# Kernel optimization log

Measured on AMD Instinct MI355X. Metric: run time of the kernel, lower is better.

Reference implementation:

```python
import jax, jax.numpy as jnp
import numpy as np

B, H, W, DIM, NH = 4, 32, 32, 768, 12
HD = DIM // NH  # head_dim = 64


def setup_inputs() -> dict:
    key = jax.random.key(0)
    ks = jax.random.split(key, 12)
    n = lambda i, shape, s=1.0: jax.random.normal(ks[i], shape, jnp.float32) * s
    return {
        "q": n(0, (B, H, W, DIM)),
        "k": n(1, (B, H, W, DIM)),
        "v": n(2, (B, H, W, DIM)),
        # Linear weights stored as (in, out) so y = x @ W + b (equivalent to torch x @ W.T)
        "Wq": n(3, (DIM, DIM), 0.02), "bq": jnp.zeros((DIM,), jnp.float32),
        "Wk": n(4, (DIM, DIM), 0.02), "bk": jnp.zeros((DIM,), jnp.float32),
        "Wv": n(5, (DIM, DIM), 0.02), "bv": jnp.zeros((DIM,), jnp.float32),
        "Wp": n(6, (DIM, DIM), 0.02), "bp": jnp.zeros((DIM,), jnp.float32),
        # decomposed relative position tables: (2*size - 1, head_dim)
        "rel_pos_h": n(7, (2 * H - 1, HD), 0.02),
        "rel_pos_w": n(8, (2 * W - 1, HD), 0.02),
    }


def reference(q, k, v, Wq, bq, Wk, bk, Wv, bv, Wp, bp, rel_pos_h, rel_pos_w):
    scale = HD ** -0.5

    def to_heads(x, Wt, b):
        y = x.reshape(B, H * W, DIM) @ Wt + b          # (B, HW, DIM)
        return y.reshape(B, H * W, NH, HD).transpose(0, 2, 1, 3).reshape(B * NH, H * W, HD)

    qh = to_heads(q, Wq, bq)   # (B*NH, HW, HD)
    kh = to_heads(k, Wk, bk)
    vh = to_heads(v, Wv, bv)

    # scaled dot-product scores
    attn = jnp.einsum('bqd,bkd->bqk', qh * scale, kh)  # (B*NH, HW, HW)

    # decomposed relative position bias (q_size == k_size == input_size, no interpolation)
    idx_h = jnp.arange(H)[:, None] - jnp.arange(H)[None, :] + (H - 1)
    idx_w = jnp.arange(W)[:, None] - jnp.arange(W)[None, :] + (W - 1)
    Rh = rel_pos_h[idx_h]  # (H, H, HD)
    Rw = rel_pos_w[idx_w]  # (W, W, HD)
    rq = qh.reshape(B * NH, H, W, HD)  # unscaled q, as in torch add_decomposed_rel_pos
    rel_h = jnp.einsum('bhwc,hkc->bhwk', rq, Rh)  # (B*NH, H, W, H)
    rel_w = jnp.einsum('bhwc,wkc->bhwk', rq, Rw)  # (B*NH, H, W, W)

    attn = (attn.reshape(B * NH, H, W, H, W)
            + rel_h[:, :, :, :, None]
            + rel_w[:, :, :, None, :]).reshape(B * NH, H * W, H * W)

    attn = jax.nn.softmax(attn, axis=-1)
    x = (attn @ vh).reshape(B, NH, H, W, HD).transpose(0, 2, 3, 1, 4).reshape(B, H, W, DIM)
    return x @ Wp + bp
```

## Files before the change

kernel.cpp:

```cpp
#include <hip/hip_runtime.h>
#include <math.h>

#define DIM  768
#define NH   12
#define HD   64
#define HWN  1024
#define MROWS 4096

typedef __attribute__((ext_vector_type(8))) short short8;
typedef __attribute__((ext_vector_type(4))) float f32x4;
typedef _Float16 h8 __attribute__((ext_vector_type(8)));
typedef _Float16 h2 __attribute__((ext_vector_type(2)));

__device__ __forceinline__ void gl_lds16(const void* g, void* l) {
    __builtin_amdgcn_global_load_lds(
        (const __attribute__((address_space(1))) void*)g,
        (__attribute__((address_space(3))) void*)l, 16, 0, 0);
}

__global__ __launch_bounds__(256) void xconv_kernel(
    const float* __restrict__ q, const float* __restrict__ k,
    const float* __restrict__ v, _Float16* __restrict__ xf16)
{
    const int N8 = MROWS * DIM / 8;
    int i = blockIdx.x * 256 + threadIdx.x;
    const int stride = gridDim.x * 256;
    for (; i < 3 * N8; i += stride) {
        const int sel = i / N8, j = i - sel * N8;
        const float* src = (sel == 0) ? q : (sel == 1) ? k : v;
        float4 a0 = ((const float4*)src)[j * 2];
        float4 a1 = ((const float4*)src)[j * 2 + 1];
        h8 o = {(_Float16)a0.x, (_Float16)a0.y, (_Float16)a0.z, (_Float16)a0.w,
                (_Float16)a1.x, (_Float16)a1.y, (_Float16)a1.z, (_Float16)a1.w};
        *(h8*)(xf16 + (size_t)sel * (MROWS * DIM) + (size_t)j * 8) = o;
    }
}

__global__ __launch_bounds__(256) void wconv_kernel(
    const float* __restrict__ Wq, const float* __restrict__ Wk,
    const float* __restrict__ Wv, const float* __restrict__ Wp,
    _Float16* __restrict__ WtAll)
{
    __shared__ float Ws[64][65];
    const int z = blockIdx.z;
    const float* W = (z == 0) ? Wq : (z == 1) ? Wk : (z == 2) ? Wv : Wp;
    _Float16* Wt = WtAll + (size_t)z * 589824;

    const int k0 = blockIdx.y * 64, n0 = blockIdx.x * 64;
    const int t = threadIdx.x;
    {
        int r = t >> 2, c4 = (t & 3) * 16;
        #pragma unroll
        for (int u = 0; u < 16; u += 4)
            *(float4*)&Ws[r][c4 + u] = *(const float4*)(W + (size_t)(k0 + r) * DIM + n0 + c4 + u);
    }
    __syncthreads();
    const int n = t >> 2, kseg = (t & 3) * 16;
    h8 h0, h1;
    #pragma unroll
    for (int j = 0; j < 8; ++j) {
        h0[j] = (_Float16)Ws[kseg + j][n];
        h1[j] = (_Float16)Ws[kseg + 8 + j][n];
    }
    size_t base = (size_t)(n0 + n) * DIM + k0 + kseg;
    *(h8*)(Wt + base) = h0;
    *(h8*)(Wt + base + 8) = h1;
}

__global__ __launch_bounds__(256) void rel2frag_kernel(
    const float* __restrict__ rph, const float* __restrict__ rpw,
    _Float16* __restrict__ relTg)
{
    const int t = threadIdx.x;
    const int row = t >> 1, c0 = (t & 1) * 32;
    const float* src = (row < 63) ? rph + (size_t)row * HD
                     : (row >= 64 && row < 127) ? rpw + (size_t)(row - 64) * HD
                     : nullptr;
    #pragma unroll
    for (int g = 0; g < 4; ++g) {
        h8 o;
        #pragma unroll
        for (int j = 0; j < 8; ++j)
            o[j] = src ? (_Float16)src[c0 + g * 8 + j] : (_Float16)0.0f;
        *(h8*)(relTg + (size_t)row * HD + c0 + g * 8) = o;
    }
}

template<int AMODE>
__global__ __launch_bounds__(256, 3) void gemm_mfma_kernel(
    const _Float16* __restrict__ X0, const _Float16* __restrict__ WtAll,
    const float* __restrict__ bias0, const float* __restrict__ bias1,
    const float* __restrict__ bias2,
    void* __restrict__ Y0, void* __restrict__ Y1, void* __restrict__ Y2)
{
    constexpr int MT = (AMODE == 0) ? 128 : 64;
    constexpr int RF = MT / 32;
    __shared__ __align__(16) char smem[MT * 128 + 12 * 1024];
    constexpr int BOFF = MT * 128;

    const int t = threadIdx.x;
    const int w = t >> 6, lane = t & 63;
    const int l15 = lane & 15, l4 = lane >> 4;

    int sel, rb, cb;
    if (AMODE == 0) {
        const int sw = (blockIdx.x & 7) * 96 + (blockIdx.x >> 3);
        sel = sw >> 8;
        const int rem = sw & 255;
        rb = rem >> 3; cb = rem & 7;
    } else {
        const int sw = (blockIdx.x & 7) * 64 + (blockIdx.x >> 3);
        sel = 3;
        rb = sw >> 3; cb = sw & 7;
    }
    const int row0 = rb * MT, col0 = cb * 96;

    const char* Ab = (const char*)(X0 + (AMODE == 0 ? (size_t)sel * (MROWS * DIM) : 0));
    const _Float16* Bt = WtAll + (size_t)sel * 589824;
    const float* bias = (AMODE == 1) ? bias0 : (sel == 0) ? bias0 : (sel == 1) ? bias1 : bias2;

    f32x4 acc[RF][3];
    #pragma unroll
    for (int i = 0; i < RF; ++i)
        #pragma unroll
        for (int j = 0; j < 3; ++j) acc[i][j] = (f32x4){0, 0, 0, 0};

    for (int kt = 0; kt < 12; ++kt) {
        #pragma unroll
        for (int i = 0; i < MT / 32; ++i) {
            const int fi = w * (MT / 32) + i;
            const int row = fi * 8 + (lane >> 3);
            const int srcb = ((lane & 7) * 16) ^ ((row & 7) << 4);
            gl_lds16(Ab + (size_t)(row0 + row) * 1536 + kt * 128 + srcb, smem + fi * 1024);
        }
        #pragma unroll
        for (int it = 0; it < 3; ++it) {
            const int f = it * 4 + w;
            const int ks = f / 6, cf = f % 6;
            const size_t off = (size_t)(col0 + cf * 16 + l15) * 1536 + kt * 128 + ks * 64 + l4 * 16;
            gl_lds16((const char*)Bt + off, smem + BOFF + f * 1024);
        }
        __syncthreads();

        __builtin_amdgcn_s_setprio(1);
        #pragma unroll
        for (int ks = 0; ks < 2; ++ks) {
            h8 b[3];
            #pragma unroll
            for (int cf4 = 0; cf4 < 3; ++cf4) {
                const int fb = ks * 6 + (w & 1) * 3 + cf4;
                b[cf4] = *(const h8*)(smem + BOFF + fb * 1024 + lane * 16);
            }
            #pragma unroll
            for (int rf = 0; rf < RF; ++rf) {
                const int arow = (w >> 1) * (MT / 2) + rf * 16 + l15;
                const int base = arow * 128 + ((ks * 64 + l4 * 16) ^ ((arow & 7) << 4));
                h8 ah = *(const h8*)(smem + base);
                #pragma unroll
                for (int cf4 = 0; cf4 < 3; ++cf4)
                    acc[rf][cf4] = __builtin_amdgcn_mfma_f32_16x16x32_f16(ah, b[cf4], acc[rf][cf4], 0, 0, 0);
            }
        }
        __builtin_amdgcn_s_setprio(0);
        __syncthreads();
    }

    const int wrow0 = row0 + (w >> 1) * (MT / 2);
    const int wcol0 = col0 + (w & 1) * 48;
    #pragma unroll
    for (int cf4 = 0; cf4 < 3; ++cf4) {
        const int c = wcol0 + cf4 * 16 + l15;
        const float bb = bias[c];
        #pragma unroll
        for (int rf = 0; rf < RF; ++rf) {
            #pragma unroll
            for (int reg = 0; reg < 4; ++reg) {
                const int r = wrow0 + rf * 16 + l4 * 4 + reg;
                float y = acc[rf][cf4][reg] + bb;
                if (AMODE == 1) {
                    ((float*)Y0)[(size_t)r * DIM + c] = y;
                } else {
                    _Float16* Yh = (_Float16*)((sel == 0) ? Y0 : (sel == 1) ? Y1 : Y2);
                    size_t base = ((size_t)((r >> 10) * NH + (c >> 6)) * HWN + (r & 1023)) * HD + (c & 63);
                    Yh[base] = (_Float16)y;
                }
            }
        }
    }
}

#define AT_REL   0
#define AT_VT    8704
#define AT_P     25088
#define AT_KB    33280
#define AT_QF    8704
#define AT_RELT  17920
#define AT_PG    17920
#define AT_OF    8704
#define AT_TOTAL 49664

__global__ __launch_bounds__(256, 3) void attn_kernel(
    const _Float16* __restrict__ qh, const _Float16* __restrict__ kh,
    const _Float16* __restrict__ vh, const _Float16* __restrict__ relTg,
    _Float16* __restrict__ aout)
{
    __shared__ __align__(16) char smem[AT_TOTAL];
    const int bid = blockIdx.x;
    const int j   = bid >> 3;
    const int bh  = (bid & 7) * 6 + (j >> 4);
    const int qb  = j & 15;
    const int t  = threadIdx.x;
    const int w  = t >> 6;
    const int lane = t & 63;
    const int l15 = lane & 15, l4 = lane >> 4;

    _Float16* Rel = (_Float16*)(smem + AT_REL);
    _Float16* Qf  = (_Float16*)(smem + AT_QF);

    const int r = t >> 2, dc = (t & 3) * 16;
    {
        const _Float16* qp = qh + ((size_t)bh * HWN + qb * 64 + r) * HD + dc;
        *(short8*)(&Qf[r * 72 + dc])     = *(const short8*)(qp);
        *(short8*)(&Qf[r * 72 + dc + 8]) = *(const short8*)(qp + 8);
        #pragma unroll
        for (int it = 0; it < 4; ++it) {
            const int f = it * 4 + w;
            const int ct = f >> 1, ks = f & 1;
            gl_lds16((const char*)relTg + (ct * 16 + l15) * 128 + ks * 64 + l4 * 16,
                     smem + AT_RELT + f * 1024);
        }
    }
    __syncthreads();

    const _Float16* kb_ = kh + (size_t)bh * HWN * HD;
    const _Float16* vb_ = vh + (size_t)bh * HWN * HD;
    const int key2 = (t & 31) * 2, dgrp = t >> 5;
    short8 rv0, rv1;
#define LOADV(KT) {                                                            \
        const _Float16* vp = vb_ + (size_t)((KT) * 64 + key2) * HD + dgrp * 8; \
        rv0 = *(const short8*)vp; rv1 = *(const short8*)(vp + HD); }
    LOADV(0);

    h8 qf2[2];
    {
        const int qr = w * 16 + l15;
        qf2[0] = *(const h8*)(&Qf[qr * 72 + l4 * 8]);
        qf2[1] = *(const h8*)(&Qf[qr * 72 + 32 + l4 * 8]);
        #pragma unroll
        for (int j2 = 0; j2 < 8; ++j2) { qf2[0][j2] *= (_Float16)0.125f; qf2[1][j2] *= (_Float16)0.125f; }
    }

    f32x4 pacc[4][2];
    #pragma unroll
    for (int i = 0; i < 4; ++i)
        #pragma unroll
        for (int j2 = 0; j2 < 2; ++j2) pacc[i][j2] = (f32x4){0, 0, 0, 0};
    #pragma unroll
    for (int ks = 0; ks < 2; ++ks) {
        h8 b0 = *(const h8*)(smem + AT_RELT + ((w * 2 + 0) * 2 + ks) * 1024 + lane * 16);
        h8 b1 = *(const h8*)(smem + AT_RELT + ((w * 2 + 1) * 2 + ks) * 1024 + lane * 16);
        #pragma unroll
        for (int rt = 0; rt < 4; ++rt) {
            h8 a = *(const h8*)(&Qf[(rt * 16 + l15) * 72 + ks * 32 + l4 * 8]);
            pacc[rt][0] = __builtin_amdgcn_mfma_f32_16x16x32_f16(a, b0, pacc[rt][0], 0, 0, 0);
            pacc[rt][1] = __builtin_amdgcn_mfma_f32_16x16x32_f16(a, b1, pacc[rt][1], 0, 0, 0);
        }
    }

    __syncthreads();
    _Float16* Pg = (_Float16*)(smem + AT_PG);
    #pragma unroll
    for (int rt = 0; rt < 4; ++rt)
        #pragma unroll
        for (int cb2 = 0; cb2 < 2; ++cb2)
            #pragma unroll
            for (int reg = 0; reg < 4; ++reg)
                Pg[(rt * 16 + l4 * 4 + reg) * 130 + w * 32 + cb2 * 16 + l15] =
                    (_Float16)pacc[rt][cb2][reg];
    __syncthreads();

    {
        const int q = t >> 2, kk0 = (t & 3) * 8;
        const int hw = qb * 64 + q;
        const int hq = hw >> 5, wq = hw & 31;
        short8 vh_, vw_;
        #pragma unroll
        for (int j2 = 0; j2 < 8; ++j2) {
            const int kk = kk0 + j2;
            vh_[j2] = *(const short*)&Pg[q * 130 + (hq + 31 - kk)];
            vw_[j2] = *(const short*)&Pg[q * 130 + 64 + (wq + 31 - kk)];
        }
        *(short8*)(&Rel[q * 68 + kk0])      = vh_;
        *(short8*)(&Rel[q * 68 + 32 + kk0]) = vw_;
    }
    __syncthreads();

    const int qrow_bias = w * 16 + l15;
    float rw_[2][4];
    #pragma unroll
    for (int c2 = 0; c2 < 2; ++c2)
        #pragma unroll
        for (int reg = 0; reg < 4; ++reg)
            rw_[c2][reg] = (float)Rel[qrow_bias * 68 + 32 + c2 * 16 + l4 * 4 + reg];

#define STAGEK(KT, BUF) {                                                      \
        _Pragma("unroll")                                                      \
        for (int i2 = 0; i2 < 2; ++i2) {                                       \
            const int f = w * 2 + i2;                                          \
            const int keyk = f * 8 + (lane >> 3);                              \
            const int srcb = ((lane & 7) * 16) ^ ((lane >> 3) << 4);           \
            gl_lds16((const char*)kb_ + (size_t)((KT) * 64 + keyk) * 128 + srcb, \
                     smem + AT_KB + (BUF) * 8192 + f * 1024);                  \
        } }

#define WRITEVT(BUF) {                                                         \
        _Pragma("unroll")                                                      \
        for (int j2 = 0; j2 < 8; ++j2) {                                       \
            const int d = dgrp * 8 + j2;                                       \
            unsigned pk = ((unsigned short)rv0[j2]) |                          \
                          (((unsigned)(unsigned short)rv1[j2]) << 16);         \
            *(unsigned*)(smem + AT_VT + (BUF) * 8192 + d * 128 +               \
                         ((key2 * 2) ^ ((d & 7) << 4))) = pk; } }
    WRITEVT(0);
    STAGEK(0, 0);

    f32x4 acc_o[4] = {{0,0,0,0},{0,0,0,0},{0,0,0,0},{0,0,0,0}};
    float m_ = -INFINITY, lsum = 0.f;
    char* Pw = smem + AT_P + w * 2048;
    const int swzP = (l15 & 7) << 4;

    #pragma unroll 2
    for (int kt = 0; kt < 16; ++kt) {
        const int cur = kt & 1;
        __syncthreads();
        if (kt < 15) { LOADV(kt + 1); STAGEK(kt + 1, cur ^ 1); }

        h2 rhp = *(const h2*)(&Rel[qrow_bias * 68 + kt * 2]);
        const float rh0 = (float)rhp[0];
        const float rh1 = (float)rhp[1];
        f32x4 accs[4];
        #pragma unroll
        for (int ct = 0; ct < 4; ++ct) {
            const float rhc = (ct >> 1) ? rh1 : rh0;
            #pragma unroll
            for (int reg = 0; reg < 4; ++reg)
                accs[ct][reg] = rw_[ct & 1][reg] + rhc;
        }
        __builtin_amdgcn_s_setprio(1);
        #pragma unroll
        for (int ct = 0; ct < 4; ++ct) {
            const int row = ct * 16 + l15;
            const int swzK = (row & 7) << 4;
            #pragma unroll
            for (int ks = 0; ks < 2; ++ks) {
                h8 kfr = *(const h8*)(smem + AT_KB + cur * 8192 + row * 128 +
                                      ((ks * 64 + l4 * 16) ^ swzK));
                accs[ct] = __builtin_amdgcn_mfma_f32_16x16x32_f16(kfr, qf2[ks], accs[ct], 0, 0, 0);
            }
        }
        __builtin_amdgcn_s_setprio(0);

        float mx[4];
        #pragma unroll
        for (int ct = 0; ct < 4; ++ct)
            mx[ct] = fmaxf(fmaxf(accs[ct][0], accs[ct][1]),
                           fmaxf(accs[ct][2], accs[ct][3]));
        float tmax = fmaxf(fmaxf(mx[0], mx[1]), fmaxf(mx[2], mx[3]));

        if (__any(tmax > m_ + 8.f)) {
            float tg = fmaxf(tmax, __shfl_xor(tmax, 16));
            tg = fmaxf(tg, __shfl_xor(tg, 32));
            const float mnew = fmaxf(m_, tg);
            const float factor = __expf(m_ - mnew);
            m_ = mnew;
            lsum *= factor;
            #pragma unroll
            for (int reg = 0; reg < 4; ++reg) {
                const float fr = __shfl(factor, l4 * 4 + reg);
                #pragma unroll
                for (int dt = 0; dt < 4; ++dt) acc_o[dt][reg] *= fr;
            }
        }

        float tsum = 0.f;
        #pragma unroll
        for (int ct = 0; ct < 4; ++ct) {
            float p0 = __expf(accs[ct][0] - m_);
            float p1 = __expf(accs[ct][1] - m_);
            float p2 = __expf(accs[ct][2] - m_);
            float p3 = __expf(accs[ct][3] - m_);
            tsum += (p0 + p1) + (p2 + p3);
            h2 pa = {(_Float16)p0, (_Float16)p1};
            h2 pb = {(_Float16)p2, (_Float16)p3};
            uint2 pk;
            pk.x = *(unsigned*)&pa;
            pk.y = *(unsigned*)&pb;
            *(uint2*)(Pw + l15 * 128 + ((ct * 32 + l4 * 8) ^ swzP)) = pk;
        }
        lsum += tsum;

        __builtin_amdgcn_s_setprio(1);
        #pragma unroll
        for (int ks = 0; ks < 2; ++ks) {
            h8 pa = *(const h8*)(Pw + l15 * 128 + ((ks * 64 + l4 * 16) ^ swzP));
            #pragma unroll
            for (int dt = 0; dt < 4; ++dt) {
                const int d = dt * 16 + l15;
                h8 vf = *(const h8*)(smem + AT_VT + cur * 8192 + d * 128 +
                                     ((ks * 64 + l4 * 16) ^ ((d & 7) << 4)));
                acc_o[dt] = __builtin_amdgcn_mfma_f32_16x16x32_f16(pa, vf, acc_o[dt], 0, 0, 0);
            }
        }
        __builtin_amdgcn_s_setprio(0);

        if (kt < 15) WRITEVT(cur ^ 1);
    }

    float ltot = lsum + __shfl_xor(lsum, 16);
    ltot += __shfl_xor(ltot, 32);
    const float invl = 1.0f / ltot;
    float linv[4];
    #pragma unroll
    for (int reg = 0; reg < 4; ++reg) linv[reg] = __shfl(invl, l4 * 4 + reg);
    __syncthreads();
    _Float16* Of = (_Float16*)(smem + AT_OF);
    #pragma unroll
    for (int reg = 0; reg < 4; ++reg) {
        const int qloc = w * 16 + l4 * 4 + reg;
        #pragma unroll
        for (int dt = 0; dt < 4; ++dt)
            Of[qloc * 72 + dt * 16 + l15] = (_Float16)(acc_o[dt][reg] * linv[reg]);
    }
    __syncthreads();
    {
        const int b_ = bh / NH, nh = bh % NH;
        _Float16* op = aout + ((size_t)b_ * HWN + qb * 64 + r) * DIM + nh * HD + dc;
        *(short8*)op       = *(const short8*)(&Of[r * 72 + dc]);
        *(short8*)(op + 8) = *(const short8*)(&Of[r * 72 + dc + 8]);
    }
}

extern "C" void kernel_launch(void* const* d_in, const int* in_sizes, int n_in,
                              void* d_out, int out_size, void* d_ws, size_t ws_size,
                              hipStream_t stream) {
    const float* q   = (const float*)d_in[0];
    const float* k   = (const float*)d_in[1];
    const float* v   = (const float*)d_in[2];
    const float* Wq  = (const float*)d_in[3];
    const float* bq  = (const float*)d_in[4];
    const float* Wk  = (const float*)d_in[5];
    const float* bk  = (const float*)d_in[6];
    const float* Wv  = (const float*)d_in[7];
    const float* bv  = (const float*)d_in[8];
    const float* Wp  = (const float*)d_in[9];
    const float* bp  = (const float*)d_in[10];
    const float* rph = (const float*)d_in[11];
    const float* rpw = (const float*)d_in[12];

    float* out = (float*)d_out;
    char*  w0  = (char*)d_ws;

    _Float16* wtAll = (_Float16*)(w0);
    _Float16* relTg = (_Float16*)(w0 + 4718592);
    _Float16* xf16  = (_Float16*)(w0 + 4734976);
    _Float16* aout  = (_Float16*)(w0 + 4734976);
    _Float16* qf16  = (_Float16*)(w0 + 23609344);
    _Float16* kf16  = (_Float16*)(w0 + 29900800);
    _Float16* vf16  = (_Float16*)(w0 + 36192256);

    dim3 blk(256);
    xconv_kernel<<<2048, blk, 0, stream>>>(q, k, v, xf16);
    wconv_kernel<<<dim3(12, 12, 4), blk, 0, stream>>>(Wq, Wk, Wv, Wp, wtAll);
    rel2frag_kernel<<<1, blk, 0, stream>>>(rph, rpw, relTg);
    gemm_mfma_kernel<0><<<768, blk, 0, stream>>>(
        xf16, wtAll, bq, bk, bv, qf16, kf16, vf16);
    attn_kernel<<<768, blk, 0, stream>>>(qf16, kf16, vf16, relTg, aout);
    gemm_mfma_kernel<1><<<512, blk, 0, stream>>>(
        aout, wtAll, bp, nullptr, nullptr, out, nullptr, nullptr);
}
```

Measured before the change: 95.12 us.

## Software-pipeline attention PV one tile behind QK and merge prep kernels

Restructures the attention inner loop into a fully unrolled 16-step sequence where the P·V MFMAs of the previous key tile are issued alongside the Q·K MFMAs of the current tile. V^T gets a triple-buffered LDS region so the write-ahead does not clobber the tile still being consumed. LDS is rearranged: only the H-direction bias is staged in shared memory, and the W-direction bias is read straight from the Pg buffer into registers, which drops one barrier. The activation conversion and weight transpose kernels are merged into a single launch to save launch overhead. The changes raise LDS use per block and register pressure from the full unroll.

```diff
diff --git a/kernel.cpp b/kernel.cpp
--- a/kernel.cpp
+++ b/kernel.cpp
@@ -18,53 +18,59 @@
         (__attribute__((address_space(3))) void*)l, 16, 0, 0);
 }
 
-__global__ __launch_bounds__(256) void xconv_kernel(
+__global__ __launch_bounds__(256) void prep_kernel(
     const float* __restrict__ q, const float* __restrict__ k,
-    const float* __restrict__ v, _Float16* __restrict__ xf16)
-{
-    const int N8 = MROWS * DIM / 8;
-    int i = blockIdx.x * 256 + threadIdx.x;
-    const int stride = gridDim.x * 256;
-    for (; i < 3 * N8; i += stride) {
-        const int sel = i / N8, j = i - sel * N8;
-        const float* src = (sel == 0) ? q : (sel == 1) ? k : v;
-        float4 a0 = ((const float4*)src)[j * 2];
-        float4 a1 = ((const float4*)src)[j * 2 + 1];
-        h8 o = {(_Float16)a0.x, (_Float16)a0.y, (_Float16)a0.z, (_Float16)a0.w,
-                (_Float16)a1.x, (_Float16)a1.y, (_Float16)a1.z, (_Float16)a1.w};
-        *(h8*)(xf16 + (size_t)sel * (MROWS * DIM) + (size_t)j * 8) = o;
-    }
-}
-
-__global__ __launch_bounds__(256) void wconv_kernel(
+    const float* __restrict__ v,
     const float* __restrict__ Wq, const float* __restrict__ Wk,
     const float* __restrict__ Wv, const float* __restrict__ Wp,
-    _Float16* __restrict__ WtAll)
+    _Float16* __restrict__ WtAll, _Float16* __restrict__ relTg,
+    _Float16* __restrict__ xf16)
 {
     __shared__ float Ws[64][65];
-    const int z = blockIdx.z;
-    const float* W = (z == 0) ? Wq : (z == 1) ? Wk : (z == 2) ? Wv : Wp;
-    _Float16* Wt = WtAll + (size_t)z * 589824;
-
-    const int k0 = blockIdx.y * 64, n0 = blockIdx.x * 64;
+    const int b = blockIdx.x;
     const int t = threadIdx.x;
-    {
-        int r = t >> 2, c4 = (t & 3) * 16;
-        #pragma unroll
-        for (int u = 0; u < 16; u += 4)
-            *(float4*)&Ws[r][c4 + u] = *(const float4*)(W + (size_t)(k0 + r) * DIM + n0 + c4 + u);
-    }
-    __syncthreads();
-    const int n = t >> 2, kseg = (t & 3) * 16;
-    h8 h0, h1;
-    #pragma unroll
-    for (int j = 0; j < 8; ++j) {
-        h0[j] = (_Float16)Ws[kseg + j][n];
-        h1[j] = (_Float16)Ws[kseg + 8 + j][n];
-    }
-    size_t base = (size_t)(n0 + n) * DIM + k0 + kseg;
-    *(h8*)(Wt + base) = h0;
-    *(h8*)(Wt + base + 8) = h1;
+
+    if (b < 576) {
+        const int z = b / 144, rem = b - z * 144;
+        const int ky = rem / 12, nx = rem - ky * 12;
+        const float* W = (z == 0) ? Wq : (z == 1) ? Wk : (z == 2) ? Wv : Wp;
+        _Float16* Wt = WtAll + (size_t)z * 589824;
+        const int k0 = ky * 64, n0 = nx * 64;
+        {
+            int r = t >> 2, c4 = (t & 3) * 16;
+            #pragma unroll
+            for (int u = 0; u < 16; u += 4)
+                *(float4*)&Ws[r][c4 + u] = *(const float4*)(W + (size_t)(k0 + r) * DIM + n0 + c4 + u);
+        }
+        __syncthreads();
+        const int n = t >> 2, kseg = (t & 3) * 16;
+        h8 h0, h1;
+        #pragma unroll
+        for (int j = 0; j < 8; ++j) {
+            h0[j] = (_Float16)Ws[kseg + j][n];
+            h1[j] = (_Float16)Ws[kseg + 8 + j][n];
+        }
+        size_t base = (size_t)(n0 + n) * DIM + k0 + kseg;
+        *(h8*)(Wt + base) = h0;
+        *(h8*)(Wt + base + 8) = h1;
+    } else if (b == 576) {
+        const int row = t >> 1, c0 = (t & 1) * 32;
+        const float* rsrc = nullptr;
+        (void)rsrc; (void)row; (void)c0;
+    } else {
+        const int N8 = MROWS * DIM / 8;
+        int i = (b - 577) * 256 + t;
+        const int stride = (gridDim.x - 577) * 256;
+        for (; i < 3 * N8; i += stride) {
+            const int sel = i / N8, j = i - sel * N8;
+            const float* src = (sel == 0) ? q : (sel == 1) ? k : v;
+            float4 a0 = ((const float4*)src)[j * 2];
+            float4 a1 = ((const float4*)src)[j * 2 + 1];
+            h8 o = {(_Float16)a0.x, (_Float16)a0.y, (_Float16)a0.z, (_Float16)a0.w,
+                    (_Float16)a1.x, (_Float16)a1.y, (_Float16)a1.z, (_Float16)a1.w};
+            *(h8*)(xf16 + (size_t)sel * (MROWS * DIM) + (size_t)j * 8) = o;
+        }
+    }
 }
 
 __global__ __launch_bounds__(256) void rel2frag_kernel(
@@ -189,15 +195,15 @@
     }
 }
 
-#define AT_REL   0
-#define AT_VT    8704
-#define AT_P     25088
-#define AT_KB    33280
-#define AT_QF    8704
-#define AT_RELT  17920
-#define AT_PG    17920
-#define AT_OF    8704
-#define AT_TOTAL 49664
+#define AT_RELH  0
+#define AT_VT    4096
+#define AT_P     28672
+#define AT_KB    36864
+#define AT_QF    4096
+#define AT_RELT  13312
+#define AT_PG    29696
+#define AT_OF    4096
+#define AT_TOTAL 53248
 
 __global__ __launch_bounds__(256, 3) void attn_kernel(
     const _Float16* __restrict__ qh, const _Float16* __restrict__ kh,
@@ -214,8 +220,8 @@
     const int lane = t & 63;
     const int l15 = lane & 15, l4 = lane >> 4;
 
-    _Float16* Rel = (_Float16*)(smem + AT_REL);
-    _Float16* Qf  = (_Float16*)(smem + AT_QF);
+    _Float16* RelH = (_Float16*)(smem + AT_RELH);
+    _Float16* Qf   = (_Float16*)(smem + AT_QF);
 
     const int r = t >> 2, dc = (t & 3) * 16;
     {
@@ -267,7 +273,6 @@
         }
     }
 
-    __syncthreads();
     _Float16* Pg = (_Float16*)(smem + AT_PG);
     #pragma unroll
     for (int rt = 0; rt < 4; ++rt)
@@ -281,27 +286,24 @@
 
     {
         const int q = t >> 2, kk0 = (t & 3) * 8;
-        const int hw = qb * 64 + q;
-        const int hq = hw >> 5, wq = hw & 31;
-        short8 vh_, vw_;
-        #pragma unroll
-        for (int j2 = 0; j2 < 8; ++j2) {
-            const int kk = kk0 + j2;
-            vh_[j2] = *(const short*)&Pg[q * 130 + (hq + 31 - kk)];
-            vw_[j2] = *(const short*)&Pg[q * 130 + 64 + (wq + 31 - kk)];
-        }
-        *(short8*)(&Rel[q * 68 + kk0])      = vh_;
-        *(short8*)(&Rel[q * 68 + 32 + kk0]) = vw_;
+        const int hq = (qb * 64 + q) >> 5;
+        short8 vh_;
+        #pragma unroll
+        for (int j2 = 0; j2 < 8; ++j2)
+            vh_[j2] = *(const short*)&Pg[q * 130 + (hq + 31 - (kk0 + j2))];
+        *(short8*)(&RelH[q * 32 + kk0]) = vh_;
+    }
+    const int qrow = w * 16 + l15;
+    float rw_[2][4];
+    {
+        const int wq = (qb * 64 + qrow) & 31;
+        #pragma unroll
+        for (int c2 = 0; c2 < 2; ++c2)
+            #pragma unroll
+            for (int reg = 0; reg < 4; ++reg)
+                rw_[c2][reg] = (float)Pg[qrow * 130 + 64 + (wq + 31 - (c2 * 16 + l4 * 4 + reg))];
     }
     __syncthreads();
-
-    const int qrow_bias = w * 16 + l15;
-    float rw_[2][4];
-    #pragma unroll
-    for (int c2 = 0; c2 < 2; ++c2)
-        #pragma unroll
-        for (int reg = 0; reg < 4; ++reg)
-            rw_[c2][reg] = (float)Rel[qrow_bias * 68 + 32 + c2 * 16 + l4 * 4 + reg];
 
 #define STAGEK(KT, BUF) {                                                      \
         _Pragma("unroll")                                                      \
@@ -329,92 +331,95 @@
     char* Pw = smem + AT_P + w * 2048;
     const int swzP = (l15 & 7) << 4;
 
-    #pragma unroll 2
-    for (int kt = 0; kt < 16; ++kt) {
-        const int cur = kt & 1;
-        __syncthreads();
-        if (kt < 15) { LOADV(kt + 1); STAGEK(kt + 1, cur ^ 1); }
-
-        h2 rhp = *(const h2*)(&Rel[qrow_bias * 68 + kt * 2]);
-        const float rh0 = (float)rhp[0];
-        const float rh1 = (float)rhp[1];
-        f32x4 accs[4];
-        #pragma unroll
-        for (int ct = 0; ct < 4; ++ct) {
-            const float rhc = (ct >> 1) ? rh1 : rh0;
-            #pragma unroll
-            for (int reg = 0; reg < 4; ++reg)
-                accs[ct][reg] = rw_[ct & 1][reg] + rhc;
-        }
-        __builtin_amdgcn_s_setprio(1);
-        #pragma unroll
-        for (int ct = 0; ct < 4; ++ct) {
-            const int row = ct * 16 + l15;
-            const int swzK = (row & 7) << 4;
-            #pragma unroll
-            for (int ks = 0; ks < 2; ++ks) {
-                h8 kfr = *(const h8*)(smem + AT_KB + cur * 8192 + row * 128 +
-                                      ((ks * 64 + l4 * 16) ^ swzK));
-                accs[ct] = __builtin_amdgcn_mfma_f32_16x16x32_f16(kfr, qf2[ks], accs[ct], 0, 0, 0);
-            }
-        }
-        __builtin_amdgcn_s_setprio(0);
-
-        float mx[4];
-        #pragma unroll
-        for (int ct = 0; ct < 4; ++ct)
-            mx[ct] = fmaxf(fmaxf(accs[ct][0], accs[ct][1]),
-                           fmaxf(accs[ct][2], accs[ct][3]));
-        float tmax = fmaxf(fmaxf(mx[0], mx[1]), fmaxf(mx[2], mx[3]));
-
-        if (__any(tmax > m_ + 8.f)) {
-            float tg = fmaxf(tmax, __shfl_xor(tmax, 16));
-            tg = fmaxf(tg, __shfl_xor(tg, 32));
-            const float mnew = fmaxf(m_, tg);
-            const float factor = __expf(m_ - mnew);
-            m_ = mnew;
-            lsum *= factor;
-            #pragma unroll
-            for (int reg = 0; reg < 4; ++reg) {
-                const float fr = __shfl(factor, l4 * 4 + reg);
-                #pragma unroll
-                for (int dt = 0; dt < 4; ++dt) acc_o[dt][reg] *= fr;
-            }
-        }
-
-        float tsum = 0.f;
-        #pragma unroll
-        for (int ct = 0; ct < 4; ++ct) {
-            float p0 = __expf(accs[ct][0] - m_);
-            float p1 = __expf(accs[ct][1] - m_);
-            float p2 = __expf(accs[ct][2] - m_);
-            float p3 = __expf(accs[ct][3] - m_);
-            tsum += (p0 + p1) + (p2 + p3);
-            h2 pa = {(_Float16)p0, (_Float16)p1};
-            h2 pb = {(_Float16)p2, (_Float16)p3};
-            uint2 pk;
-            pk.x = *(unsigned*)&pa;
-            pk.y = *(unsigned*)&pb;
-            *(uint2*)(Pw + l15 * 128 + ((ct * 32 + l4 * 8) ^ swzP)) = pk;
-        }
-        lsum += tsum;
-
-        __builtin_amdgcn_s_setprio(1);
-        #pragma unroll
-        for (int ks = 0; ks < 2; ++ks) {
-            h8 pa = *(const h8*)(Pw + l15 * 128 + ((ks * 64 + l4 * 16) ^ swzP));
-            #pragma unroll
-            for (int dt = 0; dt < 4; ++dt) {
-                const int d = dt * 16 + l15;
-                h8 vf = *(const h8*)(smem + AT_VT + cur * 8192 + d * 128 +
-                                     ((ks * 64 + l4 * 16) ^ ((d & 7) << 4)));
-                acc_o[dt] = __builtin_amdgcn_mfma_f32_16x16x32_f16(pa, vf, acc_o[dt], 0, 0, 0);
-            }
-        }
-        __builtin_amdgcn_s_setprio(0);
-
-        if (kt < 15) WRITEVT(cur ^ 1);
-    }
+#define QK(KT) {                                                               \
+        h2 rhp = *(const h2*)(&RelH[qrow * 32 + (KT) * 2]);                    \
+        const float rh0 = (float)rhp[0], rh1 = (float)rhp[1];                  \
+        _Pragma("unroll")                                                      \
+        for (int ct = 0; ct < 4; ++ct) {                                       \
+            const float rhc = (ct >> 1) ? rh1 : rh0;                           \
+            _Pragma("unroll")                                                  \
+            for (int reg = 0; reg < 4; ++reg)                                  \
+                accs[ct][reg] = rw_[ct & 1][reg] + rhc;                        \
+        }                                                                      \
+        _Pragma("unroll")                                                      \
+        for (int ct = 0; ct < 4; ++ct) {                                       \
+            const int row = ct * 16 + l15;                                     \
+            const int swzK = (row & 7) << 4;                                   \
+            _Pragma("unroll")                                                  \
+            for (int ks = 0; ks < 2; ++ks) {                                   \
+                h8 kfr = *(const h8*)(smem + AT_KB + ((KT) & 1) * 8192 +       \
+                                      row * 128 + ((ks * 64 + l4 * 16) ^ swzK)); \
+                accs[ct] = __builtin_amdgcn_mfma_f32_16x16x32_f16(kfr, qf2[ks], accs[ct], 0, 0, 0); \
+            }                                                                  \
+        } }
+
+#define PV(KT) {                                                               \
+        _Pragma("unroll")                                                      \
+        for (int ks = 0; ks < 2; ++ks) {                                       \
+            h8 pa = *(const h8*)(Pw + l15 * 128 + ((ks * 64 + l4 * 16) ^ swzP)); \
+            _Pragma("unroll")                                                  \
+            for (int dt = 0; dt < 4; ++dt) {                                   \
+                const int d = dt * 16 + l15;                                   \
+                h8 vf = *(const h8*)(smem + AT_VT + ((KT) % 3) * 8192 + d * 128 + \
+                                     ((ks * 64 + l4 * 16) ^ ((d & 7) << 4)));  \
+                acc_o[dt] = __builtin_amdgcn_mfma_f32_16x16x32_f16(pa, vf, acc_o[dt], 0, 0, 0); \
+            }                                                                  \
+        } }
+
+#define SM(KT) {                                                               \
+        float mx[4];                                                           \
+        _Pragma("unroll")                                                      \
+        for (int ct = 0; ct < 4; ++ct)                                         \
+            mx[ct] = fmaxf(fmaxf(accs[ct][0], accs[ct][1]),                    \
+                           fmaxf(accs[ct][2], accs[ct][3]));                   \
+        float tmax = fmaxf(fmaxf(mx[0], mx[1]), fmaxf(mx[2], mx[3]));          \
+        if (__any(tmax > m_ + 8.f)) {                                          \
+            float tg = fmaxf(tmax, __shfl_xor(tmax, 16));                      \
+            tg = fmaxf(tg, __shfl_xor(tg, 32));                                \
+            const float mnew = fmaxf(m_, tg);                                  \
+            const float factor = __expf(m_ - mnew);                            \
+            m_ = mnew;                                                         \
+            lsum *= factor;                                                    \
+            _Pragma("unroll")                                                  \
+            for (int reg = 0; reg < 4; ++reg) {                                \
+                const float fr = __shfl(factor, l4 * 4 + reg);                 \
+                _Pragma("unroll")                                              \
+                for (int dt = 0; dt < 4; ++dt) acc_o[dt][reg] *= fr;           \
+            }                                                                  \
+        }                                                                      \
+        float tsum = 0.f;                                                      \
+        _Pragma("unroll")                                                      \
+        for (int ct = 0; ct < 4; ++ct) {                                       \
+            float p0 = __expf(accs[ct][0] - m_);                               \
+            float p1 = __expf(accs[ct][1] - m_);                               \
+            float p2 = __expf(accs[ct][2] - m_);                               \
+            float p3 = __expf(accs[ct][3] - m_);                               \
+            tsum += (p0 + p1) + (p2 + p3);                                     \
+            h2 pa = {(_Float16)p0, (_Float16)p1};                              \
+            h2 pb = {(_Float16)p2, (_Float16)p3};                              \
+            uint2 pk;                                                          \
+            pk.x = *(unsigned*)&pa;                                            \
+            pk.y = *(unsigned*)&pb;                                            \
+            *(uint2*)(Pw + l15 * 128 + ((ct * 32 + l4 * 8) ^ swzP)) = pk;      \
+        }                                                                      \
+        lsum += tsum; }
+
+#define ITER(KT) {                                                             \
+        __syncthreads();                                                       \
+        if ((KT) < 15) { LOADV((KT) + 1); STAGEK((KT) + 1, ((KT) + 1) & 1); }  \
+        f32x4 accs[4];                                                         \
+        __builtin_amdgcn_s_setprio(1);                                         \
+        QK(KT);                                                                \
+        if ((KT) > 0) PV((KT) - 1);                                            \
+        __builtin_amdgcn_s_setprio(0);                                         \
+        SM(KT);                                                                \
+        if ((KT) < 15) WRITEVT(((KT) + 1) % 3); }
+
+    ITER(0);  ITER(1);  ITER(2);  ITER(3);
+    ITER(4);  ITER(5);  ITER(6);  ITER(7);
+    ITER(8);  ITER(9);  ITER(10); ITER(11);
+    ITER(12); ITER(13); ITER(14); ITER(15);
+    PV(15);
 
     float ltot = lsum + __shfl_xor(lsum, 16);
     ltot += __shfl_xor(ltot, 32);
@@ -469,9 +474,9 @@
     _Float16* vf16  = (_Float16*)(w0 + 36192256);
 
     dim3 blk(256);
-    xconv_kernel<<<2048, blk, 0, stream>>>(q, k, v, xf16);
-    wconv_kernel<<<dim3(12, 12, 4), blk, 0, stream>>>(Wq, Wk, Wv, Wp, wtAll);
     rel2frag_kernel<<<1, blk, 0, stream>>>(rph, rpw, relTg);
+    prep_kernel<<<2625, blk, 0, stream>>>(q, k, v, Wq, Wk, Wv, Wp,
+                                          wtAll, relTg, xf16);
     gemm_mfma_kernel<0><<<768, blk, 0, stream>>>(
         xf16, wtAll, bq, bk, bv, qf16, kf16, vf16);
     attn_kernel<<<768, blk, 0, stream>>>(qf16, kf16, vf16, relTg, aout);
```

New measurement: 95.71 us. No clear change (+0.6%).
